# Optimization experiments

Hardware: AMD Instinct MI355X
Metric: run time of the kernel (lower is better)

Reference implementation:

```python
import jax, jax.numpy as jnp
import numpy as np

D_MODEL = 1024
N_HEADS = 16
DEPTH = D_MODEL // N_HEADS  # 64
GATE_DIM = 512
B, S = 2, 2048


def setup_inputs() -> dict:
    key = jax.random.key(0)
    ks = jax.random.split(key, 16)
    sd = lambda fan_in: 1.0 / np.sqrt(fan_in)
    inp = {
        "v": jax.random.normal(ks[0], (B, S, D_MODEL), jnp.float32),
        "k": jax.random.normal(ks[1], (B, S, D_MODEL), jnp.float32),
        "q": jax.random.normal(ks[2], (B, S, D_MODEL), jnp.float32),
        # padding mask: 1.0 => masked out (added as -1e9)
        "mask": (jax.random.uniform(ks[3], (B, 1, 1, S)) < 0.1).astype(jnp.float32),
        "Wq": jax.random.normal(ks[4], (D_MODEL, D_MODEL), jnp.float32) * sd(D_MODEL),
        "bq": jnp.zeros((D_MODEL,), jnp.float32),
        "Wk": jax.random.normal(ks[5], (D_MODEL, D_MODEL), jnp.float32) * sd(D_MODEL),
        "bk": jnp.zeros((D_MODEL,), jnp.float32),
        "Wv": jax.random.normal(ks[6], (D_MODEL, D_MODEL), jnp.float32) * sd(D_MODEL),
        "bv": jnp.zeros((D_MODEL,), jnp.float32),
        "Wgk": jax.random.normal(ks[7], (DEPTH, GATE_DIM), jnp.float32) * sd(DEPTH),
        "bgk": jnp.zeros((GATE_DIM,), jnp.float32),
        "Wgq": jax.random.normal(ks[8], (DEPTH, GATE_DIM), jnp.float32) * sd(DEPTH),
        "bgq": jnp.zeros((GATE_DIM,), jnp.float32),
        "Wm": jax.random.normal(ks[9], (GATE_DIM, 2), jnp.float32) * sd(GATE_DIM),
        "bm": jnp.zeros((2,), jnp.float32),
        "Wo": jax.random.normal(ks[10], (D_MODEL, D_MODEL), jnp.float32) * sd(D_MODEL),
        "bo": jnp.zeros((D_MODEL,), jnp.float32),
    }
    return inp


def _split_heads(x):
    # (B, S, d_model) -> (B, H, S, depth)
    b, s, _ = x.shape
    return x.reshape(b, s, N_HEADS, DEPTH).transpose(0, 2, 1, 3)


def reference(v, k, q, mask, Wq, bq, Wk, bk, Wv, bv,
              Wgk, bgk, Wgq, bgq, Wm, bm, Wo, bo):
    qh = _split_heads(q @ Wq + bq)  # (B,H,S,D)
    kh = _split_heads(k @ Wk + bk)
    vh = _split_heads(v @ Wv + bv)

    # gated scaled dot-product attention (is_self=True path, gate_dim=512)
    gk = kh @ Wgk + bgk                      # (B,H,S,512)
    gq = qh @ Wgq + bgq                      # (B,H,S,512)
    M = jax.nn.sigmoid((gk * gq) @ Wm + bm)  # (B,H,S,2)
    qh = qh * M[..., 0:1]
    kh = kh * M[..., 1:2]

    scale = 1.0 / jnp.sqrt(jnp.float32(DEPTH))
    logits = jnp.einsum("bhqd,bhkd->bhqk", qh, kh) * scale
    logits = logits + mask * -1e9
    attn = jax.nn.softmax(logits, axis=-1)           # (B,H,Sq,Sk)
    out = jnp.einsum("bhqk,bhkd->bhqd", attn, vh)    # (B,H,S,D)

    out = out.transpose(0, 2, 1, 3).reshape(out.shape[0], -1, D_MODEL)
    out = out @ Wo + bo
    return out, attn
```

## Files before the change

### kernel.cpp

```cpp
#include <hip/hip_runtime.h>
#include <hip/hip_bf16.h>
#include <cstdint>
#include <cstddef>

typedef __attribute__((ext_vector_type(8))) short short8;
typedef __attribute__((ext_vector_type(4))) short short4v;
typedef __attribute__((ext_vector_type(4))) float f32x4;

#define M4      4194304ull
#define OUT_ELE 4194304ull

static __device__ __forceinline__ short f2bf(float f) {
  __hip_bfloat16 h = __float2bfloat16(f);
  union { __hip_bfloat16 b; short s; } u; u.b = h; return u.s;
}
static __device__ __forceinline__ float bf2f(short s) {
  union { short s; __hip_bfloat16 b; } u; u.s = s; return __bfloat162float(u.b);
}
static __device__ __forceinline__ void split2(float v, short &hi, short &lo) {
  hi = f2bf(v);
  lo = f2bf(v - bf2f(hi));
}

typedef void __attribute__((address_space(1)))* gas1_t;
typedef void __attribute__((address_space(3)))* las3_t;
static __device__ __forceinline__ void gload16(const void* g, void* l) {
  __builtin_amdgcn_global_load_lds((gas1_t)(void*)g, (las3_t)l, 16, 0, 0);
}

__global__ void k_split_inputs(const float* __restrict__ q, const float* __restrict__ k,
                               const float* __restrict__ v,
                               short* __restrict__ xh, short* __restrict__ xl) {
  int z = blockIdx.y;
  const float* src = (z == 0) ? q : ((z == 1) ? k : v);
  size_t i = ((size_t)blockIdx.x * blockDim.x + threadIdx.x) * 4;
  float4 f = *(const float4*)(src + i);
  size_t o = (size_t)z * M4 + i;
  short h0,l0,h1,l1,h2,l2,h3,l3;
  split2(f.x,h0,l0); split2(f.y,h1,l1); split2(f.z,h2,l2); split2(f.w,h3,l3);
  short4v hv = {h0,h1,h2,h3}, lv = {l0,l1,l2,l3};
  *(short4v*)(xh + o) = hv;
  *(short4v*)(xl + o) = lv;
}

__global__ void k_prep_w(const float* __restrict__ Wq, const float* __restrict__ Wk,
                         const float* __restrict__ Wv, const float* __restrict__ Wo,
                         short* __restrict__ wth, short* __restrict__ wtl) {
  int z = blockIdx.z;
  const float* W = (z==0)?Wq:((z==1)?Wk:((z==2)?Wv:Wo));
  __shared__ float tile[32][33];
  int n0 = blockIdx.x * 32, k0 = blockIdx.y * 32;
  int tx = threadIdx.x & 31, ty = threadIdx.x >> 5;
  #pragma unroll
  for (int s = 0; s < 4; ++s)
    tile[ty + 8*s][tx] = W[(size_t)(k0 + ty + 8*s) * 1024 + n0 + tx];
  __syncthreads();
  size_t zb = (size_t)z * 1048576;
  #pragma unroll
  for (int s = 0; s < 4; ++s) {
    float vv = tile[tx][ty + 8*s];
    short hi, lo; split2(vv, hi, lo);
    size_t idx = zb + (size_t)(n0 + ty + 8*s) * 1024 + k0 + tx;
    wth[idx] = hi; wtl[idx] = lo;
  }
}

__global__ void k_gateprep(const float* __restrict__ Wgk, const float* __restrict__ Wgq,
                           const float* __restrict__ Wm,
                           const float* __restrict__ bgk, const float* __restrict__ bgq,
                           const float* __restrict__ bm,
                           float* __restrict__ A, float* __restrict__ U,
                           float* __restrict__ Wvec, float* __restrict__ Cc) {
  int t = blockIdx.x / 65;
  int d = blockIdx.x % 65;
  bool isW = (d == 64);
  __shared__ float T[128 * 65];
  __shared__ float sj[512];
  __shared__ float red[256];
  int tid = threadIdx.x;
  for (int j = tid; j < 512; j += 256)
    sj[j] = Wm[(size_t)j * 2 + t] * (isW ? bgk[j] : Wgk[(size_t)d * 512 + j]);
  __syncthreads();
  int grp = tid >> 6, e = tid & 63;
  float acc = 0.f;
  for (int c = 0; c < 4; ++c) {
    int j0 = c * 128;
    __syncthreads();
    for (int it = 0; it < 32; ++it) {
      int lin = it * 256 + tid;
      int jj = lin & 127, ee = lin >> 7;
      T[jj * 65 + ee] = Wgq[(size_t)ee * 512 + j0 + jj];
    }
    __syncthreads();
    for (int jj = grp * 32; jj < grp * 32 + 32; ++jj)
      acc = fmaf(sj[j0 + jj], T[jj * 65 + e], acc);
  }
  red[tid] = acc;
  __syncthreads();
  if (grp == 0) {
    float r = red[e] + red[64 + e] + red[128 + e] + red[192 + e];
    if (isW) Wvec[t * 64 + e] = r;
    else     A[(size_t)t * 4096 + d * 64 + e] = r;
  }
  if (tid == 0) {
    float s = 0.f;
    for (int j = 0; j < 512; ++j) s += sj[j] * bgq[j];
    if (isW) Cc[t] = s + bm[t];
    else     U[t * 64 + d] = s;
  }
}

template<int EPI>
__global__ __launch_bounds__(256) void k_gemm(
    const short* __restrict__ Ah_g, const short* __restrict__ Al_g,
    const short* __restrict__ Bh_g, const short* __restrict__ Bl_g,
    const float* __restrict__ b0, const float* __restrict__ b1, const float* __restrict__ b2,
    float* __restrict__ Cout, short* __restrict__ Oh, short* __restrict__ Ol) {
  const int K = 1024;
  int z = blockIdx.z;
  const short* Ah = Ah_g + (size_t)z * M4;
  const short* Al = Al_g + (size_t)z * M4;
  const short* Bh = Bh_g + (size_t)z * 1048576;
  const short* Bl = Bl_g + (size_t)z * 1048576;
  const float* bias = (z == 0) ? b0 : ((z == 1) ? b1 : b2);
  int m0 = blockIdx.y * 128, n0 = blockIdx.x * 128;
  __shared__ __align__(16) short As_h[4096], As_l[4096], Bs_h[4096], Bs_l[4096];
  int tid = threadIdx.x;
  int l = tid & 63, w = tid >> 6;
  int wr = w >> 1, wc = w & 1;
  int ar = l & 15, ko = (l >> 4) * 8;
  f32x4 acc[4][4];
  #pragma unroll
  for (int m = 0; m < 4; ++m)
    #pragma unroll
    for (int n = 0; n < 4; ++n) acc[m][n] = {0.f,0.f,0.f,0.f};
  for (int kk = 0; kk < K; kk += 32) {
    __syncthreads();
    #pragma unroll
    for (int p = 0; p < 2; ++p) {
      int g = p * 256 + tid;
      int row = g >> 2, gc = (g & 3) * 8;
      size_t as = (size_t)(m0 + row) * K + kk + gc;
      size_t bs = (size_t)(n0 + row) * K + kk + gc;
      int ldb = g * 16;
      gload16(&Ah[as], (char*)As_h + ldb);
      gload16(&Al[as], (char*)As_l + ldb);
      gload16(&Bh[bs], (char*)Bs_h + ldb);
      gload16(&Bl[bs], (char*)Bs_l + ldb);
    }
    __syncthreads();
    short8 aH[4], aL[4], bH[4], bL[4];
    #pragma unroll
    for (int m = 0; m < 4; ++m) {
      int r = (wr * 64 + m * 16 + ar) * 32 + ko;
      aH[m] = *(short8*)&As_h[r];
      aL[m] = *(short8*)&As_l[r];
    }
    #pragma unroll
    for (int n = 0; n < 4; ++n) {
      int r = (wc * 64 + n * 16 + ar) * 32 + ko;
      bH[n] = *(short8*)&Bs_h[r];
      bL[n] = *(short8*)&Bs_l[r];
    }
    #pragma unroll
    for (int m = 0; m < 4; ++m)
      #pragma unroll
      for (int n = 0; n < 4; ++n) {
        acc[m][n] = __builtin_amdgcn_mfma_f32_16x16x32_bf16(aH[m], bH[n], acc[m][n], 0, 0, 0);
        acc[m][n] = __builtin_amdgcn_mfma_f32_16x16x32_bf16(aH[m], bL[n], acc[m][n], 0, 0, 0);
        acc[m][n] = __builtin_amdgcn_mfma_f32_16x16x32_bf16(aL[m], bH[n], acc[m][n], 0, 0, 0);
      }
  }
  #pragma unroll
  for (int m = 0; m < 4; ++m)
    #pragma unroll
    for (int n = 0; n < 4; ++n)
      #pragma unroll
      for (int i = 0; i < 4; ++i) {
        int row = m0 + wr * 64 + m * 16 + (l >> 4) * 4 + i;
        int col = n0 + wc * 64 + n * 16 + ar;
        float vv = acc[m][n][i] + bias[col];
        if (EPI == 1) {
          Cout[(size_t)row * 1024 + col] = vv;
        } else {
          int b = row >> 11, s = row & 2047, h = col >> 6, dd = col & 63;
          size_t idx = (size_t)z * M4 + (((size_t)(b * 16 + h)) * 2048 + s) * 64 + dd;
          short hi, lo; split2(vv, hi, lo);
          Oh[idx] = hi; Ol[idx] = lo;
        }
      }
}

__global__ void k_vt(const short* __restrict__ vh_h, const short* __restrict__ vh_l,
                     short* __restrict__ vt_h, short* __restrict__ vt_l) {
  int s0 = blockIdx.x * 64, bh = blockIdx.y;
  __shared__ short th[64][65], tl[64][65];
  int tid = threadIdx.x;
  int c = tid & 63, r4 = tid >> 6;
  #pragma unroll
  for (int s = 0; s < 16; ++s) {
    int r = r4 * 16 + s;
    size_t src = ((size_t)bh * 2048 + s0 + r) * 64 + c;
    th[r][c] = vh_h[src]; tl[r][c] = vh_l[src];
  }
  __syncthreads();
  #pragma unroll
  for (int s = 0; s < 16; ++s) {
    int dd = r4 * 16 + s;
    size_t dst = ((size_t)bh * 64 + dd) * 2048 + s0 + c;
    vt_h[dst] = th[c][dd]; vt_l[dst] = tl[c][dd];
  }
}

__global__ void k_gate(short* __restrict__ qh_h, short* __restrict__ qh_l,
                       short* __restrict__ kh_h, short* __restrict__ kh_l,
                       const float* __restrict__ A, const float* __restrict__ U,
                       const float* __restrict__ Wvec, const float* __restrict__ Cc) {
  __shared__ float A0s[4096], A1s[4096];
  __shared__ float rowk[4][64];
  int tid = threadIdx.x, w = tid >> 6, l = tid & 63;
  for (int i = tid; i < 4096; i += 256) { A0s[i] = A[i]; A1s[i] = A[4096 + i]; }
  __syncthreads();
  float u0 = U[l], u1 = U[64 + l];
  float w0 = Wvec[l], w1 = Wvec[64 + l];
  float c0 = Cc[0], c1 = Cc[1];
  for (int rr = 0; rr < 16; ++rr) {
    size_t row = (size_t)blockIdx.x * 64 + w * 16 + rr;
    size_t base = row * 64 + l;
    float qv = bf2f(qh_h[base]) + bf2f(qh_l[base]);
    float kv = bf2f(kh_h[base]) + bf2f(kh_l[base]);
    rowk[w][l] = kv;
    float y0 = 0.f, y1 = 0.f;
    for (int dd = 0; dd < 64; ++dd) {
      float kd = rowk[w][dd];
      y0 = fmaf(kd, A0s[dd * 64 + l], y0);
      y1 = fmaf(kd, A1s[dd * 64 + l], y1);
    }
    float p0 = y0 * qv + u0 * kv + w0 * qv;
    float p1 = y1 * qv + u1 * kv + w1 * qv;
    #pragma unroll
    for (int mm = 1; mm < 64; mm <<= 1) { p0 += __shfl_xor(p0, mm); p1 += __shfl_xor(p1, mm); }
    p0 += c0; p1 += c1;
    float M0 = 1.f / (1.f + expf(-p0));
    float M1 = 1.f / (1.f + expf(-p1));
    short hi, lo;
    split2(qv * M0, hi, lo); qh_h[base] = hi; qh_l[base] = lo;
    split2(kv * M1, hi, lo); kh_h[base] = hi; kh_l[base] = lo;
  }
}

__global__ __launch_bounds__(512, 4) void k_attn(
    const short* __restrict__ ph_h, const short* __restrict__ ph_l,
    const short* __restrict__ vt_h, const short* __restrict__ vt_l,
    const float* __restrict__ mask,
    float* __restrict__ attn, short* __restrict__ mh_h, short* __restrict__ mh_l) {
  int bid = blockIdx.x;
  int xcd = bid & 7, slot = bid >> 3;
  int bh = (xcd << 2) | (slot >> 4);
  int s0 = (slot & 15) << 7;
  int b = bh >> 4, h = bh & 15;
  int tid = threadIdx.x, w = tid >> 6, l = tid & 63;
  int ar = l & 15, hi4 = l >> 4, a7 = ar & 7;
  __shared__ __align__(16) short Ksh[2][4096];
  __shared__ __align__(16) short Ksl[2][4096];
  __shared__ __align__(16) short Vsh[4096];
  __shared__ __align__(16) short Vsl[4096];
  __shared__ __align__(16) short Pb[8][1024];
  __shared__ short maskb[2048];
  for (int i = tid; i < 2048; i += 512)
    maskb[i] = f2bf(mask[(size_t)b * 2048 + i] * -1e9f);

  const short* kh_h = ph_h + M4;
  const short* kh_l = ph_l + M4;
  const char* gKh = (const char*)kh_h + (size_t)bh * 2048 * 128;
  const char* gKl = (const char*)kh_l + (size_t)bh * 2048 * 128;
  const char* gVh = (const char*)vt_h + (size_t)bh * 64 * 4096;
  const char* gVl = (const char*)vt_l + (size_t)bh * 64 * 4096;

  int rowbase = s0 + w * 16;
  size_t qbase = ((size_t)bh * 2048 + rowbase + ar) * 64 + (size_t)hi4 * 8;
  short8 aH0 = *(const short8*)&ph_h[qbase];
  short8 aH1 = *(const short8*)&ph_h[qbase + 32];
  short8 aL0 = *(const short8*)&ph_l[qbase];
  short8 aL1 = *(const short8*)&ph_l[qbase + 32];

  #define STAGE_K(tile, buf) {                                          \
    const char* th_ = gKh + (size_t)(tile) * 8192;                      \
    const char* tl_ = gKl + (size_t)(tile) * 8192;                      \
    int col_ = tid >> 3, j_ = tid & 7;                                  \
    int gs_ = col_ * 128 + ((j_ ^ (col_ & 7)) << 4);                    \
    gload16(th_ + gs_, (char*)&Ksh[buf][0] + tid * 16);                 \
    gload16(tl_ + gs_, (char*)&Ksl[buf][0] + tid * 16);                 \
  }

  #define STAGE_V(tile) {                                               \
    int row_ = tid >> 3, j_ = tid & 7;                                  \
    int gs_ = row_ * 4096 + (tile) * 128 + ((j_ ^ (row_ & 7)) << 4);    \
    gload16(gVh + gs_, (char*)Vsh + tid * 16);                          \
    gload16(gVl + gs_, (char*)Vsl + tid * 16);                          \
  }

  #define QKT(buf, tile) {                                              \
    const char* kbh_ = (const char*)&Ksh[buf][0];                       \
    const char* kbl_ = (const char*)&Ksl[buf][0];                       \
    _Pragma("unroll")                                                   \
    for (int n = 0; n < 4; ++n) {                                       \
      int colloc = n * 16 + ar;                                         \
      int cb = colloc * 128;                                            \
      short8 bH0 = *(const short8*)(kbh_ + cb + ((hi4 ^ a7) << 4));     \
      short8 bH1 = *(const short8*)(kbh_ + cb + (((hi4 + 4) ^ a7) << 4));\
      short8 bL0 = *(const short8*)(kbl_ + cb + ((hi4 ^ a7) << 4));     \
      short8 bL1 = *(const short8*)(kbl_ + cb + (((hi4 + 4) ^ a7) << 4));\
      f32x4 c = {0.f,0.f,0.f,0.f};                                      \
      c = __builtin_amdgcn_mfma_f32_16x16x32_bf16(aH0, bH0, c, 0,0,0);  \
      c = __builtin_amdgcn_mfma_f32_16x16x32_bf16(aH1, bH1, c, 0,0,0);  \
      c = __builtin_amdgcn_mfma_f32_16x16x32_bf16(aH0, bL0, c, 0,0,0);  \
      c = __builtin_amdgcn_mfma_f32_16x16x32_bf16(aH1, bL1, c, 0,0,0);  \
      c = __builtin_amdgcn_mfma_f32_16x16x32_bf16(aL0, bH0, c, 0,0,0);  \
      c = __builtin_amdgcn_mfma_f32_16x16x32_bf16(aL1, bH1, c, 0,0,0);  \
      float mv = bf2f(maskb[(tile) * 64 + colloc]);                     \
      _Pragma("unroll")                                                 \
      for (int i = 0; i < 4; ++i) lg[n][i] = c[i] * 0.125f + mv;        \
    } }

  float ls[4] = {0.f, 0.f, 0.f, 0.f};

  STAGE_K(0, 0);
  #pragma unroll 1
  for (int t = 0; t < 32; ++t) {
    __syncthreads();
    STAGE_K((t + 1) & 31, (t + 1) & 1);
    f32x4 lg[4];
    QKT(t & 1, t);
    #pragma unroll
    for (int n = 0; n < 4; ++n)
      #pragma unroll
      for (int i = 0; i < 4; ++i) ls[i] += __expf(lg[n][i]);
  }
  #pragma unroll
  for (int mk = 1; mk < 16; mk <<= 1)
    #pragma unroll
    for (int i = 0; i < 4; ++i) ls[i] += __shfl_xor(ls[i], mk);
  float invl[4];
  #pragma unroll
  for (int i = 0; i < 4; ++i) invl[i] = 1.f / ls[i];

  f32x4 acc[4];
  #pragma unroll
  for (int dn = 0; dn < 4; ++dn) acc[dn] = {0.f,0.f,0.f,0.f};
  size_t arow = (size_t)bh * 2048 + rowbase;

  #pragma unroll 1
  for (int t = 0; t < 32; ++t) {
    __syncthreads();
    STAGE_V(t);
    if (t < 31) STAGE_K(t + 1, (t + 1) & 1);
    f32x4 lg[4];
    QKT(t & 1, t);
    char* pbw = (char*)&Pb[w][0];
    #pragma unroll
    for (int n = 0; n < 4; ++n) {
      #pragma unroll
      for (int i = 0; i < 4; ++i) {
        float p = __expf(lg[n][i]) * invl[i];
        lg[n][i] = p;
        int r = hi4 * 4 + i;
        int off = (r * 128 + (n * 16 + ar) * 2) ^ ((r & 7) << 4);
        *(short*)(pbw + off) = f2bf(p);
      }
    }
    asm volatile("s_waitcnt vmcnt(0)" ::: "memory");
    __builtin_amdgcn_s_barrier();
    __builtin_amdgcn_sched_barrier(0);
    #pragma unroll
    for (int ks = 0; ks < 2; ++ks) {
      int roff = (ar * 128 + ks * 64 + hi4 * 16) ^ (a7 << 4);
      short8 pah = *(const short8*)(pbw + roff);
      #pragma unroll
      for (int dn = 0; dn < 4; ++dn) {
        int voff = (dn * 16 + ar) * 128 + ((ks * 64 + hi4 * 16) ^ (a7 << 4));
        short8 vH = *(const short8*)((const char*)Vsh + voff);
        short8 vL = *(const short8*)((const char*)Vsl + voff);
        acc[dn] = __builtin_amdgcn_mfma_f32_16x16x32_bf16(pah, vH, acc[dn], 0,0,0);
        acc[dn] = __builtin_amdgcn_mfma_f32_16x16x32_bf16(pah, vL, acc[dn], 0,0,0);
      }
    }
    #pragma unroll
    for (int n = 0; n < 4; ++n)
      #pragma unroll
      for (int i = 0; i < 4; ++i)
        __builtin_nontemporal_store(lg[n][i],
            &attn[(arow + hi4 * 4 + i) * 2048 + t * 64 + n * 16 + ar]);
  }
  #pragma unroll
  for (int dn = 0; dn < 4; ++dn)
    #pragma unroll
    for (int i = 0; i < 4; ++i) {
      short hh, ll; split2(acc[dn][i], hh, ll);
      size_t idx = ((size_t)b * 2048 + rowbase + hi4 * 4 + i) * 1024
                 + h * 64 + dn * 16 + ar;
      mh_h[idx] = hh; mh_l[idx] = ll;
    }
  #undef STAGE_K
  #undef STAGE_V
  #undef QKT
}

extern "C" void kernel_launch(void* const* d_in, const int* in_sizes, int n_in,
                              void* d_out, int out_size, void* d_ws, size_t ws_size,
                              hipStream_t stream) {
  const float* v    = (const float*)d_in[0];
  const float* k    = (const float*)d_in[1];
  const float* q    = (const float*)d_in[2];
  const float* mask = (const float*)d_in[3];
  const float* Wq   = (const float*)d_in[4];
  const float* bq   = (const float*)d_in[5];
  const float* Wk   = (const float*)d_in[6];
  const float* bk   = (const float*)d_in[7];
  const float* Wv   = (const float*)d_in[8];
  const float* bv   = (const float*)d_in[9];
  const float* Wgk  = (const float*)d_in[10];
  const float* bgk  = (const float*)d_in[11];
  const float* Wgq  = (const float*)d_in[12];
  const float* bgq  = (const float*)d_in[13];
  const float* Wm   = (const float*)d_in[14];
  const float* bm   = (const float*)d_in[15];
  const float* Wo   = (const float*)d_in[16];
  const float* bo   = (const float*)d_in[17];
  float* out  = (float*)d_out;
  float* attn = out + OUT_ELE;

  short* xh = (short*)attn;
  short* xl = xh + 3 * M4;

  short* wth  = (short*)d_ws;
  short* wtl  = wth + 4 * 1048576ull;
  short* ph_h = wtl + 4 * 1048576ull;
  short* ph_l = ph_h + 3 * M4;
  short* vt_h = ph_l + 3 * M4;
  short* vt_l = vt_h + M4;
  short* mh_h = vt_l + M4;
  short* mh_l = mh_h + M4;
  float* Ag   = (float*)(mh_l + M4);
  float* Ug   = Ag + 8192;
  float* Wvec = Ug + 128;
  float* Cg   = Wvec + 128;

  k_split_inputs<<<dim3(4096, 3), 256, 0, stream>>>(q, k, v, xh, xl);
  k_prep_w<<<dim3(32, 32, 4), 256, 0, stream>>>(Wq, Wk, Wv, Wo, wth, wtl);
  k_gateprep<<<130, 256, 0, stream>>>(Wgk, Wgq, Wm, bgk, bgq, bm, Ag, Ug, Wvec, Cg);
  k_gemm<0><<<dim3(8, 32, 3), 256, 0, stream>>>(xh, xl, wth, wtl, bq, bk, bv,
                                                nullptr, ph_h, ph_l);
  k_vt<<<dim3(32, 32), 256, 0, stream>>>(ph_h + 2 * M4, ph_l + 2 * M4, vt_h, vt_l);
  k_gate<<<1024, 256, 0, stream>>>(ph_h, ph_l, ph_h + M4, ph_l + M4, Ag, Ug, Wvec, Cg);
  k_attn<<<dim3(512), 512, 0, stream>>>(ph_h, ph_l, vt_h, vt_l, mask,
                                        attn, mh_h, mh_l);
  k_gemm<1><<<dim3(8, 32, 1), 256, 0, stream>>>(mh_h, mh_l,
                                                wth + 3 * 1048576ull, wtl + 3 * 1048576ull,
                                                bo, bo, bo, out, nullptr, nullptr);
}
```

Baseline: 583.9 us.

## Fuse V transpose into projection GEMM epilogue and remap block order

The V projection GEMM now writes its output straight into the transposed (B,H,D,S) layout with 4-wide short stores, so the separate k_vt transpose kernel and its extra read/write pass over V are removed. Block indices are also remapped so that consecutive blocks walk down M within a fixed N column, aiming for better L2 reuse of weight tiles. The transposed stores are strided per lane, which may coalesce less well than the old row-major writes.

```diff
diff --git a/kernel.cpp b/kernel.cpp
--- a/kernel.cpp
+++ b/kernel.cpp
@@ -115,7 +115,8 @@
     const short* __restrict__ Ah_g, const short* __restrict__ Al_g,
     const short* __restrict__ Bh_g, const short* __restrict__ Bl_g,
     const float* __restrict__ b0, const float* __restrict__ b1, const float* __restrict__ b2,
-    float* __restrict__ Cout, short* __restrict__ Oh, short* __restrict__ Ol) {
+    float* __restrict__ Cout, short* __restrict__ Oh, short* __restrict__ Ol,
+    short* __restrict__ vt_h, short* __restrict__ vt_l) {
   const int K = 1024;
   int z = blockIdx.z;
   const short* Ah = Ah_g + (size_t)z * M4;
@@ -123,7 +124,9 @@
   const short* Bh = Bh_g + (size_t)z * 1048576;
   const short* Bl = Bl_g + (size_t)z * 1048576;
   const float* bias = (z == 0) ? b0 : ((z == 1) ? b1 : b2);
-  int m0 = blockIdx.y * 128, n0 = blockIdx.x * 128;
+  int lin = blockIdx.y * 8 + blockIdx.x;
+  int wl = (lin & 7) * 32 + (lin >> 3);
+  int m0 = (wl >> 3) * 128, n0 = (wl & 7) * 128;
   __shared__ __align__(16) short As_h[4096], As_l[4096], Bs_h[4096], Bs_l[4096];
   int tid = threadIdx.x;
   int l = tid & 63, w = tid >> 6;
@@ -174,42 +177,37 @@
   #pragma unroll
   for (int m = 0; m < 4; ++m)
     #pragma unroll
-    for (int n = 0; n < 4; ++n)
-      #pragma unroll
-      for (int i = 0; i < 4; ++i) {
-        int row = m0 + wr * 64 + m * 16 + (l >> 4) * 4 + i;
-        int col = n0 + wc * 64 + n * 16 + ar;
-        float vv = acc[m][n][i] + bias[col];
-        if (EPI == 1) {
-          Cout[(size_t)row * 1024 + col] = vv;
-        } else {
-          int b = row >> 11, s = row & 2047, h = col >> 6, dd = col & 63;
-          size_t idx = (size_t)z * M4 + (((size_t)(b * 16 + h)) * 2048 + s) * 64 + dd;
+    for (int n = 0; n < 4; ++n) {
+      int row0 = m0 + wr * 64 + m * 16 + (l >> 4) * 4;
+      int col  = n0 + wc * 64 + n * 16 + ar;
+      if (EPI == 1) {
+        #pragma unroll
+        for (int i = 0; i < 4; ++i)
+          Cout[(size_t)(row0 + i) * 1024 + col] = acc[m][n][i] + bias[col];
+      } else if (z == 2) {
+        int bq = row0 >> 11, s = row0 & 2047, hh = col >> 6, dd = col & 63;
+        size_t vb = (((size_t)(bq * 16 + hh)) * 64 + dd) * 2048 + s;
+        short4v hv, lv;
+        #pragma unroll
+        for (int i = 0; i < 4; ++i) {
+          float vv = acc[m][n][i] + bias[col];
+          short hi, lo; split2(vv, hi, lo);
+          hv[i] = hi; lv[i] = lo;
+        }
+        *(short4v*)&vt_h[vb] = hv;
+        *(short4v*)&vt_l[vb] = lv;
+      } else {
+        #pragma unroll
+        for (int i = 0; i < 4; ++i) {
+          int row = row0 + i;
+          int bq = row >> 11, s = row & 2047, hh = col >> 6, dd = col & 63;
+          size_t idx = (size_t)z * M4 + (((size_t)(bq * 16 + hh)) * 2048 + s) * 64 + dd;
+          float vv = acc[m][n][i] + bias[col];
           short hi, lo; split2(vv, hi, lo);
           Oh[idx] = hi; Ol[idx] = lo;
         }
       }
-}
-
-__global__ void k_vt(const short* __restrict__ vh_h, const short* __restrict__ vh_l,
-                     short* __restrict__ vt_h, short* __restrict__ vt_l) {
-  int s0 = blockIdx.x * 64, bh = blockIdx.y;
-  __shared__ short th[64][65], tl[64][65];
-  int tid = threadIdx.x;
-  int c = tid & 63, r4 = tid >> 6;
-  #pragma unroll
-  for (int s = 0; s < 16; ++s) {
-    int r = r4 * 16 + s;
-    size_t src = ((size_t)bh * 2048 + s0 + r) * 64 + c;
-    th[r][c] = vh_h[src]; tl[r][c] = vh_l[src];
-  }
-  __syncthreads();
-  #pragma unroll
-  for (int s = 0; s < 16; ++s) {
-    int dd = r4 * 16 + s;
-    size_t dst = ((size_t)bh * 64 + dd) * 2048 + s0 + c;
-    vt_h[dst] = th[c][dd]; vt_l[dst] = tl[c][dd];
-  }
+    }
 }
 
 __global__ void k_gate(short* __restrict__ qh_h, short* __restrict__ qh_l,
@@ -450,12 +448,12 @@
   k_prep_w<<<dim3(32, 32, 4), 256, 0, stream>>>(Wq, Wk, Wv, Wo, wth, wtl);
   k_gateprep<<<130, 256, 0, stream>>>(Wgk, Wgq, Wm, bgk, bgq, bm, Ag, Ug, Wvec, Cg);
   k_gemm<0><<<dim3(8, 32, 3), 256, 0, stream>>>(xh, xl, wth, wtl, bq, bk, bv,
-                                                nullptr, ph_h, ph_l);
-  k_vt<<<dim3(32, 32), 256, 0, stream>>>(ph_h + 2 * M4, ph_l + 2 * M4, vt_h, vt_l);
+                                                nullptr, ph_h, ph_l, vt_h, vt_l);
   k_gate<<<1024, 256, 0, stream>>>(ph_h, ph_l, ph_h + M4, ph_l + M4, Ag, Ug, Wvec, Cg);
   k_attn<<<dim3(512), 512, 0, stream>>>(ph_h, ph_l, vt_h, vt_l, mask,
                                         attn, mh_h, mh_l);
   k_gemm<1><<<dim3(8, 32, 1), 256, 0, stream>>>(mh_h, mh_l,
                                                 wth + 3 * 1048576ull, wtl + 3 * 1048576ull,
-                                                bo, bo, bo, out, nullptr, nullptr);
-}
+                                                bo, bo, bo, out, nullptr, nullptr,
+                                                nullptr, nullptr);
+}
```

New measurement: 568.8 us. -2.6%, faster.
